# Kernel tuning notes

Hardware: AMD Instinct MI355X
Metric: run time of the kernel (lower is better)

## Reference

```python
import jax, jax.numpy as jnp
import numpy as np

BITS = 4
GROUP_SIZE = 128
IN_F = 4096
OUT_F = 11008
MAXQ = (1 << BITS) - 1
PACK = 32 // BITS  # 8 values per int32 word


def setup_inputs() -> dict:
    key = jax.random.key(0)
    k1, k2, k3, k4, k5 = jax.random.split(key, 5)
    x = jax.random.normal(k1, (2, 2048, IN_F), dtype=jnp.float32)
    qweight = jax.random.randint(k2, (IN_F // PACK, OUT_F), 0, 2147483647, dtype=jnp.int32)
    qzeros = jax.random.randint(k3, (IN_F // GROUP_SIZE, OUT_F // PACK), 0, 2147483647, dtype=jnp.int32)
    scales = jax.random.uniform(k4, (IN_F // GROUP_SIZE, OUT_F), dtype=jnp.float32) * 0.01 + 1e-4
    bias = jax.random.normal(k5, (OUT_F,), dtype=jnp.float32)
    return {"x": x, "qweight": qweight, "qzeros": qzeros, "scales": scales, "bias": bias}


def _dequant_weight(qweight, qzeros, scales):
    shifts = jnp.arange(0, 32, BITS, dtype=jnp.int32)
    # unpack packed int4 weights: [K/8, N] -> [K/8, 8, N] -> [K, N]
    w = (qweight[:, None, :] >> shifts[None, :, None]) & MAXQ
    w = w.reshape(-1, qweight.shape[-1]).astype(jnp.float32)  # [K, N]
    # unpack zero points: [G, N/8] -> [G, N/8, 8] -> [G, N]
    z = (qzeros[:, :, None] >> shifts[None, None, :]) & MAXQ
    z = z.reshape(qzeros.shape[0], -1).astype(jnp.float32)  # [G, N]
    gidx = jnp.arange(w.shape[0]) // GROUP_SIZE  # [K]
    # asymmetric group-wise dequant: (q - zero) * scale
    return (w - z[gidx]) * scales[gidx].astype(jnp.float32)  # [K, N]


def reference(x, qweight, qzeros, scales, bias):
    raw_dtype = x.dtype
    W = _dequant_weight(qweight, qzeros, scales)  # [K, N] fp32
    x2 = x.astype(jnp.float32).reshape(-1, x.shape[-1])  # [M, K]
    out = x2 @ W + bias.astype(jnp.float32)  # [M, N]
    return out.astype(raw_dtype).reshape(x.shape[:-1] + (W.shape[-1],))
```

## Files before the change

kernel.cpp:

```cpp
#include <hip/hip_runtime.h>
#include <hip/hip_bf16.h>
#include <stdint.h>

#define K_DIM 4096
#define N_DIM 11008
#define GROUP 128

typedef __attribute__((ext_vector_type(8))) __bf16 bf16x8;
typedef __attribute__((ext_vector_type(4))) float f32x4;
typedef __attribute__((address_space(3))) uint8_t lds_u8;
typedef __attribute__((address_space(3))) void lds_void;
typedef __attribute__((address_space(1))) const void g_void;

static __device__ inline __bf16 f2bf(float f) { return (__bf16)f; }

__global__ __launch_bounds__(256) void cvt_x_kernel(const float* __restrict__ x,
                                                    __bf16* __restrict__ xb, int total8) {
    int t = blockIdx.x * 256 + threadIdx.x;
    if (t >= total8) return;
    f32x4 a0 = *(const f32x4*)(x + (size_t)t * 8);
    f32x4 a1 = *(const f32x4*)(x + (size_t)t * 8 + 4);
    bf16x8 v;
    #pragma unroll
    for (int j = 0; j < 4; ++j) { v[j] = f2bf(a0[j]); v[j + 4] = f2bf(a1[j]); }
    *(bf16x8*)(xb + (size_t)t * 8) = v;
}

__global__ __launch_bounds__(256) void dequant_w_kernel(const int* __restrict__ qw,
                                                        const int* __restrict__ qz,
                                                        const float* __restrict__ sc,
                                                        __bf16* __restrict__ wb) {
    const int n   = blockIdx.x * 256 + threadIdx.x;
    const int kb0 = blockIdx.y * 8;
    const int g   = blockIdx.y >> 1;
    const float s   = sc[(size_t)g * N_DIM + n];
    const float nzs = -(float)((qz[(size_t)g * (N_DIM / 8) + (n >> 3)] >> ((n & 7) * 4)) & 15) * s;
    #pragma unroll
    for (int j = 0; j < 8; ++j) {
        const int w = qw[(size_t)(kb0 + j) * N_DIM + n];
        bf16x8 v;
        #pragma unroll
        for (int b = 0; b < 8; ++b)
            v[b] = f2bf(fmaf((float)((w >> (4 * b)) & 15), s, nzs));
        *(bf16x8*)(wb + (size_t)n * K_DIM + (size_t)(kb0 + j) * 8) = v;
    }
}

#define BM2 256
#define BN2 256
#define BK2 64
#define NT  (K_DIM / BK2)

__global__ __launch_bounds__(512, 2) void gemm256_kernel(
    const __bf16* __restrict__ xb, const __bf16* __restrict__ wb,
    const float* __restrict__ bias, float* __restrict__ out)
{
    __shared__ __align__(16) __bf16 As[2][BM2 * BK2];
    __shared__ __align__(16) __bf16 Bs[2][BN2 * BK2];

    const int tid  = threadIdx.x;
    const int lane = tid & 63;
    const int wid  = tid >> 6;
    const int wm = (wid >> 2) * 128;
    const int wn = (wid & 3) * 64;

    const int bid = blockIdx.x;
    const int wg  = (bid & 7) * 86 + (bid >> 3);
    const int m0 = (wg / 43) * BM2;
    const int n0 = (wg % 43) * BN2;

    const __bf16* pa[4];
    const __bf16* pb[4];
    int chk[4];
    #pragma unroll
    for (int l = 0; l < 4; ++l) {
        const int ch  = l * 512 + tid;
        const int row = ch >> 3;
        const int g   = (ch & 7) ^ (row & 7);
        chk[l] = ch;
        pa[l] = xb + (size_t)(m0 + row) * K_DIM + g * 8;
        pb[l] = wb + (size_t)(n0 + row) * K_DIM + g * 8;
    }
    lds_u8* baseA = (lds_u8*)&As[0][0];
    lds_u8* baseB = (lds_u8*)&Bs[0][0];

    auto STAGE = [&](int buf, int kofs) {
        lds_u8* dA_ = baseA + buf * (BM2 * BK2 * 2);
        lds_u8* dB_ = baseB + buf * (BN2 * BK2 * 2);
        #pragma unroll
        for (int l = 0; l < 4; ++l)
            __builtin_amdgcn_global_load_lds((g_void*)(pa[l] + kofs),
                                             (lds_void*)(dA_ + chk[l] * 16), 16, 0, 0);
        #pragma unroll
        for (int l = 0; l < 4; ++l)
            __builtin_amdgcn_global_load_lds((g_void*)(pb[l] + kofs),
                                             (lds_void*)(dB_ + chk[l] * 16), 16, 0, 0);
    };

    const int fr  = lane & 15;
    const int fc  = lane >> 4;
    const int swz = fr & 7;
    const int col0 = (fc ^ swz) * 8;
    const int col1 = ((4 + fc) ^ swz) * 8;
    const int rowoffA = (wm + fr) * BK2;
    const int rowoffB = (wn + fr) * BK2;

    f32x4 acc[8][4];
    #pragma unroll
    for (int m = 0; m < 8; ++m)
        #pragma unroll
        for (int n = 0; n < 4; ++n) acc[m][n] = (f32x4){0.f, 0.f, 0.f, 0.f};

    STAGE(0, 0);
    STAGE(1, BK2);
    asm volatile("s_waitcnt vmcnt(8)" ::: "memory");
    __builtin_amdgcn_sched_barrier(0);
    __builtin_amdgcn_s_barrier();
    __builtin_amdgcn_sched_barrier(0);

    for (int t = 0; t < NT; ++t) {
        const int cur = t & 1;
        const __bf16* ra = &As[0][0] + cur * (BM2 * BK2) + rowoffA;
        const __bf16* rb = &Bs[0][0] + cur * (BN2 * BK2) + rowoffB;
        bf16x8 aR[8], bR[8], a2[8];

        #pragma unroll
        for (int n = 0; n < 2; ++n) {
            bR[n * 2 + 0] = *(const bf16x8*)(rb + n * 1024 + col0);
            bR[n * 2 + 1] = *(const bf16x8*)(rb + n * 1024 + col1);
        }
        #pragma unroll
        for (int m = 0; m < 4; ++m) {
            aR[m * 2 + 0] = *(const bf16x8*)(ra + m * 1024 + col0);
            aR[m * 2 + 1] = *(const bf16x8*)(ra + m * 1024 + col1);
        }
        __builtin_amdgcn_s_setprio(1);
        #pragma unroll
        for (int m = 0; m < 4; ++m)
            #pragma unroll
            for (int n = 0; n < 2; ++n)
                #pragma unroll
                for (int kk = 0; kk < 2; ++kk)
                    acc[m][n] = __builtin_amdgcn_mfma_f32_16x16x32_bf16(
                        aR[m * 2 + kk], bR[n * 2 + kk], acc[m][n], 0, 0, 0);
        __builtin_amdgcn_s_setprio(0);

        #pragma unroll
        for (int n = 2; n < 4; ++n) {
            bR[n * 2 + 0] = *(const bf16x8*)(rb + n * 1024 + col0);
            bR[n * 2 + 1] = *(const bf16x8*)(rb + n * 1024 + col1);
        }
        __builtin_amdgcn_s_setprio(1);
        #pragma unroll
        for (int m = 0; m < 4; ++m)
            #pragma unroll
            for (int n = 2; n < 4; ++n)
                #pragma unroll
                for (int kk = 0; kk < 2; ++kk)
                    acc[m][n] = __builtin_amdgcn_mfma_f32_16x16x32_bf16(
                        aR[m * 2 + kk], bR[n * 2 + kk], acc[m][n], 0, 0, 0);
        __builtin_amdgcn_s_setprio(0);

        #pragma unroll
        for (int m = 0; m < 4; ++m) {
            a2[m * 2 + 0] = *(const bf16x8*)(ra + (m + 4) * 1024 + col0);
            a2[m * 2 + 1] = *(const bf16x8*)(ra + (m + 4) * 1024 + col1);
        }
        asm volatile("s_waitcnt lgkmcnt(0)" ::: "memory");
        __builtin_amdgcn_sched_barrier(0);
        __builtin_amdgcn_s_barrier();
        __builtin_amdgcn_sched_barrier(0);
        if (t + 2 < NT) STAGE(cur, (t + 2) * BK2);

        __builtin_amdgcn_s_setprio(1);
        #pragma unroll
        for (int m = 0; m < 4; ++m)
            #pragma unroll
            for (int n = 2; n < 4; ++n)
                #pragma unroll
                for (int kk = 0; kk < 2; ++kk)
                    acc[m + 4][n] = __builtin_amdgcn_mfma_f32_16x16x32_bf16(
                        a2[m * 2 + kk], bR[n * 2 + kk], acc[m + 4][n], 0, 0, 0);
        #pragma unroll
        for (int m = 0; m < 4; ++m)
            #pragma unroll
            for (int n = 0; n < 2; ++n)
                #pragma unroll
                for (int kk = 0; kk < 2; ++kk)
                    acc[m + 4][n] = __builtin_amdgcn_mfma_f32_16x16x32_bf16(
                        a2[m * 2 + kk], bR[n * 2 + kk], acc[m + 4][n], 0, 0, 0);
        __builtin_amdgcn_s_setprio(0);

        if (t + 2 < NT) { asm volatile("s_waitcnt vmcnt(8)" ::: "memory"); }
        else            { asm volatile("s_waitcnt vmcnt(0)" ::: "memory"); }
        __builtin_amdgcn_sched_barrier(0);
        __builtin_amdgcn_s_barrier();
        __builtin_amdgcn_sched_barrier(0);
    }

    const int cn  = lane & 15;
    const int cr4 = (lane >> 4) * 4;
    #pragma unroll
    for (int n = 0; n < 4; ++n) {
        const int col = n0 + wn + n * 16 + cn;
        const float bv = bias[col];
        #pragma unroll
        for (int m = 0; m < 8; ++m) {
            const int row = m0 + wm + m * 16 + cr4;
            #pragma unroll
            for (int r = 0; r < 4; ++r)
                out[(size_t)(row + r) * N_DIM + col] = acc[m][n][r] + bv;
        }
    }
}

#define FBM 128
#define FBN 128
#define FBK 32
#define FLDSS 40
__global__ __launch_bounds__(256) void gptq_gemm_fused_kernel(
    const float* __restrict__ x, const int* __restrict__ qw, const int* __restrict__ qz,
    const float* __restrict__ sc, const float* __restrict__ bias, float* __restrict__ out)
{
    __shared__ __align__(16) __bf16 Asm[FBM][FLDSS];
    __shared__ __align__(16) __bf16 Bsm[FBN][FLDSS];
    const int tid = threadIdx.x, lane = tid & 63, wid = tid >> 6;
    const int m0 = blockIdx.y * FBM, n0 = blockIdx.x * FBN;
    const int wm = (wid >> 1) * 64, wn = (wid & 1) * 64;
    f32x4 acc[4][4];
    #pragma unroll
    for (int i = 0; i < 4; ++i)
        #pragma unroll
        for (int j = 0; j < 4; ++j) acc[i][j] = (f32x4){0.f, 0.f, 0.f, 0.f};
    const int a_m = tid >> 2, a_h = tid & 3;
    const int b_n = tid & 127, b_k8 = tid >> 7;
    const int ng = n0 + b_n, zsh = (ng & 7) * 4;
    const int fr = lane & 15, fc = lane >> 4;
    for (int k0 = 0; k0 < K_DIM; k0 += FBK) {
        const int g = k0 >> 7;
        const float* xa = x + (size_t)(m0 + a_m) * K_DIM + k0 + a_h * 8;
        f32x4 a0 = *(const f32x4*)xa;
        f32x4 a1 = *(const f32x4*)(xa + 4);
        const float* xbp = xa + (size_t)64 * K_DIM;
        f32x4 a2 = *(const f32x4*)xbp;
        f32x4 a3 = *(const f32x4*)(xbp + 4);
        const int kb = (k0 >> 3) + b_k8;
        const int w0 = qw[(size_t)kb * N_DIM + ng];
        const int w1 = qw[(size_t)(kb + 2) * N_DIM + ng];
        const float s = sc[(size_t)g * N_DIM + ng];
        const float nzs = -(float)((qz[(size_t)g * (N_DIM / 8) + (ng >> 3)] >> zsh) & 15) * s;
        __syncthreads();
        bf16x8 av0, av1;
        #pragma unroll
        for (int j = 0; j < 4; ++j) {
            av0[j] = f2bf(a0[j]); av0[j + 4] = f2bf(a1[j]);
            av1[j] = f2bf(a2[j]); av1[j + 4] = f2bf(a3[j]);
        }
        *(bf16x8*)&Asm[a_m][a_h * 8] = av0;
        *(bf16x8*)&Asm[a_m + 64][a_h * 8] = av1;
        bf16x8 bv0, bv1;
        #pragma unroll
        for (int j = 0; j < 8; ++j) {
            bv0[j] = f2bf(fmaf((float)((w0 >> (4 * j)) & 15), s, nzs));
            bv1[j] = f2bf(fmaf((float)((w1 >> (4 * j)) & 15), s, nzs));
        }
        *(bf16x8*)&Bsm[b_n][b_k8 * 8] = bv0;
        *(bf16x8*)&Bsm[b_n][(b_k8 + 2) * 8] = bv1;
        __syncthreads();
        bf16x8 af[4], bfr[4];
        #pragma unroll
        for (int i = 0; i < 4; ++i) af[i] = *(const bf16x8*)&Asm[wm + i * 16 + fr][fc * 8];
        #pragma unroll
        for (int j = 0; j < 4; ++j) bfr[j] = *(const bf16x8*)&Bsm[wn + j * 16 + fr][fc * 8];
        #pragma unroll
        for (int i = 0; i < 4; ++i)
            #pragma unroll
            for (int j = 0; j < 4; ++j)
                acc[i][j] = __builtin_amdgcn_mfma_f32_16x16x32_bf16(af[i], bfr[j], acc[i][j], 0, 0, 0);
    }
    const int cn = lane & 15, cr4 = (lane >> 4) * 4;
    #pragma unroll
    for (int j = 0; j < 4; ++j) {
        const int col = n0 + wn + j * 16 + cn;
        const float bv = bias[col];
        #pragma unroll
        for (int i = 0; i < 4; ++i) {
            const int row = m0 + wm + i * 16 + cr4;
            #pragma unroll
            for (int r = 0; r < 4; ++r)
                out[(size_t)(row + r) * N_DIM + col] = acc[i][j][r] + bv;
        }
    }
}

extern "C" void kernel_launch(void* const* d_in, const int* in_sizes, int n_in,
                              void* d_out, int out_size, void* d_ws, size_t ws_size,
                              hipStream_t stream) {
    const float* x    = (const float*)d_in[0];
    const int*   qw   = (const int*)d_in[1];
    const int*   qz   = (const int*)d_in[2];
    const float* sc   = (const float*)d_in[3];
    const float* bias = (const float*)d_in[4];
    float* out = (float*)d_out;
    const int M = in_sizes[0] / K_DIM;

    const size_t xb_bytes = (size_t)M * K_DIM * sizeof(__bf16);
    const size_t wb_bytes = (size_t)N_DIM * K_DIM * sizeof(__bf16);
    if (ws_size >= xb_bytes + wb_bytes && (M % BM2) == 0) {
        __bf16* xb = (__bf16*)d_ws;
        __bf16* wb = (__bf16*)((uint8_t*)d_ws + xb_bytes);
        const int total8 = M * K_DIM / 8;
        cvt_x_kernel<<<dim3(total8 / 256), dim3(256), 0, stream>>>(x, xb, total8);
        dequant_w_kernel<<<dim3(N_DIM / 256, K_DIM / 8 / 8), dim3(256), 0, stream>>>(qw, qz, sc, wb);
        const int nblocks = (N_DIM / BN2) * (M / BM2);
        gemm256_kernel<<<dim3(nblocks), dim3(512), 0, stream>>>(xb, wb, bias, out);
    } else {
        gptq_gemm_fused_kernel<<<dim3(N_DIM / FBN, M / FBM), dim3(256), 0, stream>>>(x, qw, qz, sc, bias, out);
    }
}
```

Before: 418.2 us.

## Reschedule GEMM main loop into ping-pong phases with split prefetch

Restructures the bf16 MFMA main loop into four compute phases separated by workgroup barriers. The global-to-LDS prefetch is split into two halves, each issued between MFMA clusters. All B fragments are loaded up front, and the A second-half loads are moved earlier. The aim is to interleave memory traffic with matrix-core work in a ping-pong style, so waves alternate between issuing loads and running MFMAs. In exchange it adds several extra s_barriers per iteration and raises register pressure from holding all of bR.

```diff
diff --git a/kernel.cpp b/kernel.cpp
--- a/kernel.cpp
+++ b/kernel.cpp
@@ -84,17 +84,19 @@
     lds_u8* baseA = (lds_u8*)&As[0][0];
     lds_u8* baseB = (lds_u8*)&Bs[0][0];
 
-    auto STAGE = [&](int buf, int kofs) {
-        lds_u8* dA_ = baseA + buf * (BM2 * BK2 * 2);
-        lds_u8* dB_ = baseB + buf * (BN2 * BK2 * 2);
-        #pragma unroll
-        for (int l = 0; l < 4; ++l)
+    auto STAGE_A = [&](int buf, int half, int kofs) {
+        lds_u8* d = baseA + buf * (BM2 * BK2 * 2);
+        #pragma unroll
+        for (int l = half * 2; l < half * 2 + 2; ++l)
             __builtin_amdgcn_global_load_lds((g_void*)(pa[l] + kofs),
-                                             (lds_void*)(dA_ + chk[l] * 16), 16, 0, 0);
-        #pragma unroll
-        for (int l = 0; l < 4; ++l)
+                                             (lds_void*)(d + chk[l] * 16), 16, 0, 0);
+    };
+    auto STAGE_B = [&](int buf, int half, int kofs) {
+        lds_u8* d = baseB + buf * (BN2 * BK2 * 2);
+        #pragma unroll
+        for (int l = half * 2; l < half * 2 + 2; ++l)
             __builtin_amdgcn_global_load_lds((g_void*)(pb[l] + kofs),
-                                             (lds_void*)(dB_ + chk[l] * 16), 16, 0, 0);
+                                             (lds_void*)(d + chk[l] * 16), 16, 0, 0);
     };
 
     const int fr  = lane & 15;
@@ -111,21 +113,23 @@
         #pragma unroll
         for (int n = 0; n < 4; ++n) acc[m][n] = (f32x4){0.f, 0.f, 0.f, 0.f};
 
-    STAGE(0, 0);
-    STAGE(1, BK2);
+    STAGE_A(0, 0, 0);   STAGE_B(0, 0, 0);   STAGE_A(0, 1, 0);   STAGE_B(0, 1, 0);
+    STAGE_A(1, 0, BK2); STAGE_B(1, 0, BK2); STAGE_A(1, 1, BK2); STAGE_B(1, 1, BK2);
     asm volatile("s_waitcnt vmcnt(8)" ::: "memory");
     __builtin_amdgcn_sched_barrier(0);
     __builtin_amdgcn_s_barrier();
     __builtin_amdgcn_sched_barrier(0);
 
-    for (int t = 0; t < NT; ++t) {
-        const int cur = t & 1;
+    for (int u = 0; u < NT; ++u) {
+        const int cur = u & 1;
         const __bf16* ra = &As[0][0] + cur * (BM2 * BK2) + rowoffA;
         const __bf16* rb = &Bs[0][0] + cur * (BN2 * BK2) + rowoffB;
-        bf16x8 aR[8], bR[8], a2[8];
-
-        #pragma unroll
-        for (int n = 0; n < 2; ++n) {
+        const int  pf  = (u + 2) * BK2;
+        const bool pfv = (u + 2) < NT;
+        bf16x8 aR[8], a2[8], bR[8];
+
+        #pragma unroll
+        for (int n = 0; n < 4; ++n) {
             bR[n * 2 + 0] = *(const bf16x8*)(rb + n * 1024 + col0);
             bR[n * 2 + 1] = *(const bf16x8*)(rb + n * 1024 + col1);
         }
@@ -134,6 +138,9 @@
             aR[m * 2 + 0] = *(const bf16x8*)(ra + m * 1024 + col0);
             aR[m * 2 + 1] = *(const bf16x8*)(ra + m * 1024 + col1);
         }
+        __builtin_amdgcn_s_barrier();
+        asm volatile("s_waitcnt lgkmcnt(0)" ::: "memory");
+        __builtin_amdgcn_sched_barrier(0);
         __builtin_amdgcn_s_setprio(1);
         #pragma unroll
         for (int m = 0; m < 4; ++m)
@@ -144,12 +151,16 @@
                     acc[m][n] = __builtin_amdgcn_mfma_f32_16x16x32_bf16(
                         aR[m * 2 + kk], bR[n * 2 + kk], acc[m][n], 0, 0, 0);
         __builtin_amdgcn_s_setprio(0);
-
-        #pragma unroll
-        for (int n = 2; n < 4; ++n) {
-            bR[n * 2 + 0] = *(const bf16x8*)(rb + n * 1024 + col0);
-            bR[n * 2 + 1] = *(const bf16x8*)(rb + n * 1024 + col1);
-        }
+        __builtin_amdgcn_s_barrier();
+
+        #pragma unroll
+        for (int m = 0; m < 4; ++m) {
+            a2[m * 2 + 0] = *(const bf16x8*)(ra + (m + 4) * 1024 + col0);
+            a2[m * 2 + 1] = *(const bf16x8*)(ra + (m + 4) * 1024 + col1);
+        }
+        __builtin_amdgcn_s_barrier();
+        asm volatile("s_waitcnt lgkmcnt(0)" ::: "memory");
+        __builtin_amdgcn_sched_barrier(0);
         __builtin_amdgcn_s_setprio(1);
         #pragma unroll
         for (int m = 0; m < 4; ++m)
@@ -160,27 +171,13 @@
                     acc[m][n] = __builtin_amdgcn_mfma_f32_16x16x32_bf16(
                         aR[m * 2 + kk], bR[n * 2 + kk], acc[m][n], 0, 0, 0);
         __builtin_amdgcn_s_setprio(0);
-
-        #pragma unroll
-        for (int m = 0; m < 4; ++m) {
-            a2[m * 2 + 0] = *(const bf16x8*)(ra + (m + 4) * 1024 + col0);
-            a2[m * 2 + 1] = *(const bf16x8*)(ra + (m + 4) * 1024 + col1);
-        }
-        asm volatile("s_waitcnt lgkmcnt(0)" ::: "memory");
-        __builtin_amdgcn_sched_barrier(0);
-        __builtin_amdgcn_s_barrier();
-        __builtin_amdgcn_sched_barrier(0);
-        if (t + 2 < NT) STAGE(cur, (t + 2) * BK2);
-
+        __builtin_amdgcn_sched_barrier(0);
+        __builtin_amdgcn_s_barrier();
+        __builtin_amdgcn_sched_barrier(0);
+
+        if (pfv) { STAGE_A(cur, 0, pf); STAGE_B(cur, 0, pf); }
+        __builtin_amdgcn_s_barrier();
         __builtin_amdgcn_s_setprio(1);
-        #pragma unroll
-        for (int m = 0; m < 4; ++m)
-            #pragma unroll
-            for (int n = 2; n < 4; ++n)
-                #pragma unroll
-                for (int kk = 0; kk < 2; ++kk)
-                    acc[m + 4][n] = __builtin_amdgcn_mfma_f32_16x16x32_bf16(
-                        a2[m * 2 + kk], bR[n * 2 + kk], acc[m + 4][n], 0, 0, 0);
         #pragma unroll
         for (int m = 0; m < 4; ++m)
             #pragma unroll
@@ -190,9 +187,22 @@
                     acc[m + 4][n] = __builtin_amdgcn_mfma_f32_16x16x32_bf16(
                         a2[m * 2 + kk], bR[n * 2 + kk], acc[m + 4][n], 0, 0, 0);
         __builtin_amdgcn_s_setprio(0);
-
-        if (t + 2 < NT) { asm volatile("s_waitcnt vmcnt(8)" ::: "memory"); }
-        else            { asm volatile("s_waitcnt vmcnt(0)" ::: "memory"); }
+        __builtin_amdgcn_s_barrier();
+
+        if (pfv) { STAGE_A(cur, 1, pf); STAGE_B(cur, 1, pf); }
+        __builtin_amdgcn_s_barrier();
+        __builtin_amdgcn_s_setprio(1);
+        #pragma unroll
+        for (int m = 0; m < 4; ++m)
+            #pragma unroll
+            for (int n = 2; n < 4; ++n)
+                #pragma unroll
+                for (int kk = 0; kk < 2; ++kk)
+                    acc[m + 4][n] = __builtin_amdgcn_mfma_f32_16x16x32_bf16(
+                        a2[m * 2 + kk], bR[n * 2 + kk], acc[m + 4][n], 0, 0, 0);
+        __builtin_amdgcn_s_setprio(0);
+        if (pfv) { asm volatile("s_waitcnt vmcnt(8)" ::: "memory"); }
+        else     { asm volatile("s_waitcnt vmcnt(0)" ::: "memory"); }
         __builtin_amdgcn_sched_barrier(0);
         __builtin_amdgcn_s_barrier();
         __builtin_amdgcn_sched_barrier(0);
```

After: 443.7 us. 1.06x slower.
